# Performance work log

Measured on AMD Instinct MI355X. Metric: run time of the kernel, lower is better.

Reference implementation:

```python
import jax, jax.numpy as jnp
import numpy as np

N = 100000
F_IN = 128
HIDDEN = 64
HEADS = 4
EPS = 1e-16
SLOPE = 0.2  # PyG GATConv default negative_slope


def gat_conv(x, src, dst, W, a_src, a_dst, b, heads, out_ch, concat, n_nodes):
    # x: [N, F]; W: [F, heads*out_ch]; a_src/a_dst: [heads, out_ch]
    h = (x @ W).reshape(n_nodes, heads, out_ch)              # [N, H, C]
    alpha_s = jnp.einsum('nhc,hc->nh', h, a_src)             # [N, H]
    alpha_d = jnp.einsum('nhc,hc->nh', h, a_dst)             # [N, H]
    e = alpha_s[src] + alpha_d[dst]                          # [E, H]
    e = jnp.where(e > 0, e, SLOPE * e)                       # leaky_relu
    # segment softmax over destination node
    m = jax.ops.segment_max(e, dst, num_segments=n_nodes)    # [N, H]
    m = jnp.where(jnp.isfinite(m), m, 0.0)                   # empty segments
    ex = jnp.exp(e - m[dst])                                 # [E, H]
    denom = jax.ops.segment_sum(ex, dst, num_segments=n_nodes)  # [N, H]
    alpha = ex / (denom[dst] + EPS)                          # [E, H]
    # weighted scatter-aggregate of source features at destinations
    msg = h[src] * alpha[:, :, None]                         # [E, H, C]
    out = jax.ops.segment_sum(msg, dst, num_segments=n_nodes)  # [N, H, C]
    if concat:
        out = out.reshape(n_nodes, heads * out_ch)
    else:
        out = out.mean(axis=1)
    return out + b


def setup_inputs() -> dict:
    key = jax.random.key(0)
    ks = jax.random.split(key, 12)
    x = jax.random.normal(ks[0], (N, F_IN), dtype=jnp.float32)
    edge_index = jax.random.randint(ks[1], (2, 1600000), 0, N, dtype=jnp.int64)
    s1 = 1.0 / np.sqrt(F_IN)
    s2 = 1.0 / np.sqrt(HIDDEN)
    return {
        'x': x,
        'edge_index': edge_index,
        'W1': jax.random.normal(ks[2], (F_IN, HIDDEN), dtype=jnp.float32) * s1,
        'a_src1': jax.random.normal(ks[3], (HEADS, HIDDEN // HEADS), dtype=jnp.float32) * s2,
        'a_dst1': jax.random.normal(ks[4], (HEADS, HIDDEN // HEADS), dtype=jnp.float32) * s2,
        'b1': jnp.zeros((HIDDEN,), dtype=jnp.float32),
        'W2': jax.random.normal(ks[5], (HIDDEN, HIDDEN), dtype=jnp.float32) * s2,
        'a_src2': jax.random.normal(ks[6], (1, HIDDEN), dtype=jnp.float32) * s2,
        'a_dst2': jax.random.normal(ks[7], (1, HIDDEN), dtype=jnp.float32) * s2,
        'b2': jnp.zeros((HIDDEN,), dtype=jnp.float32),
        'Wc': jax.random.normal(ks[8], (HIDDEN, 1), dtype=jnp.float32) * s2,
        'bc': jnp.zeros((1,), dtype=jnp.float32),
    }


def reference(x, edge_index, W1, a_src1, a_dst1, b1, W2, a_src2, a_dst2, b2, Wc, bc):
    src, dst = edge_index[0], edge_index[1]
    # dropout layers are identity in eval mode
    h = gat_conv(x, src, dst, W1, a_src1, a_dst1, b1,
                 heads=HEADS, out_ch=HIDDEN // HEADS, concat=True, n_nodes=N)
    h = jax.nn.relu(h)
    h = gat_conv(h, src, dst, W2, a_src2, a_dst2, b2,
                 heads=1, out_ch=HIDDEN, concat=False, n_nodes=N)
    h = jax.nn.relu(h)
    return h @ Wc + bc  # [N, 1]
```

## Files before the change

kernel.cpp:

```cpp
#include <hip/hip_runtime.h>
#include <hip/hip_bf16.h>


typedef __hip_bfloat16 bf16;
typedef unsigned short ushort;
typedef unsigned char uchar;
typedef __attribute__((ext_vector_type(8))) short short8;
typedef __attribute__((ext_vector_type(4))) float f32x4;

#define NN 100000
#define EE 1600000
#define BKB 9
#define BKN (1 << BKB)
#define NBK ((NN + BKN - 1) >> BKB)
#define CAP 10240
#define TILE 4096
#define EPT 16
#define NT ((EE + TILE - 1) / TILE)
#define GH 391
#define GT 782
#define BN 16
#define CHE 512

__device__ __forceinline__ float relu_np(float v) { return (v < 0.f) ? 0.f : v; }
__device__ __forceinline__ float lrelu(float v) { return v > 0.f ? v : 0.2f * v; }
__device__ __forceinline__ ushort f2bf(float f) {
    __hip_bfloat16 h = __float2bfloat16(f);
    return *reinterpret_cast<ushort*>(&h);
}
__device__ __forceinline__ float bf2f(ushort u) {
    unsigned int x = ((unsigned int)u) << 16;
    return __uint_as_float(x);
}

__device__ __forceinline__ void gemm1_body(
    int gb, ushort* wB, ushort* wE,
    const float* __restrict__ x, const float* __restrict__ W1,
    const float* __restrict__ aS, const float* __restrict__ aD,
    ushort* __restrict__ h1, float* __restrict__ as1, float* __restrict__ ad1)
{
    const int tid = threadIdx.x;
    for (int i = tid; i < 128 * 64; i += 256) {
        int k = i >> 6, n = i & 63;
        wB[n * 128 + k] = f2bf(W1[i]);
    }
    for (int i = tid; i < 128 * 16; i += 256) {
        int k = i >> 4, j = i & 15;
        float v = 0.f;
        if (j < 8) {
            int h = j & 3;
            const float* av = (j < 4) ? aS : aD;
            for (int c = 0; c < 16; ++c)
                v = fmaf(W1[k * 64 + h * 16 + c], av[h * 16 + c], v);
        }
        wE[j * 128 + k] = f2bf(v);
    }
    __syncthreads();
    const int w = tid >> 6, lane = tid & 63;
    const int m = lane & 15, quad = lane >> 4;
    const int ntiles = NN >> 4;
    for (int tile = gb * 4 + w; tile < ntiles; tile += GT * 4) {
        const int row0 = tile << 4;
        f32x4 acc[4] = {f32x4{0,0,0,0}, f32x4{0,0,0,0},
                        f32x4{0,0,0,0}, f32x4{0,0,0,0}};
        f32x4 acc5 = {0, 0, 0, 0};
        const float* xp = x + (size_t)(row0 + m) * 128 + quad * 8;
        #pragma unroll
        for (int ks = 0; ks < 128; ks += 32) {
            f32x4 x0 = *(const f32x4*)(xp + ks);
            f32x4 x1 = *(const f32x4*)(xp + ks + 4);
            short8 a;
            #pragma unroll
            for (int j = 0; j < 4; ++j) a[j] = (short)f2bf(x0[j]);
            #pragma unroll
            for (int j = 0; j < 4; ++j) a[4 + j] = (short)f2bf(x1[j]);
            #pragma unroll
            for (int t = 0; t < 4; ++t) {
                short8 b = *(const short8*)&wB[(t * 16 + m) * 128 + ks + quad * 8];
                acc[t] = __builtin_amdgcn_mfma_f32_16x16x32_bf16(a, b, acc[t], 0, 0, 0);
            }
            short8 b5 = *(const short8*)&wE[m * 128 + ks + quad * 8];
            acc5 = __builtin_amdgcn_mfma_f32_16x16x32_bf16(a, b5, acc5, 0, 0, 0);
        }
        #pragma unroll
        for (int t = 0; t < 4; ++t)
            #pragma unroll
            for (int r = 0; r < 4; ++r)
                h1[(size_t)(row0 + quad * 4 + r) * 64 + t * 16 + m] = f2bf(acc[t][r]);
        #pragma unroll
        for (int r = 0; r < 4; ++r) {
            int row = row0 + quad * 4 + r;
            if (m < 4) as1[row * 4 + m] = acc5[r];
            else if (m < 8) ad1[row * 4 + (m - 4)] = acc5[r];
        }
    }
}

__global__ __launch_bounds__(256) void k_pg(
    const int* __restrict__ src, const int* __restrict__ dst,
    int* __restrict__ gcur, int* __restrict__ pairs,
    const float* __restrict__ x, const float* __restrict__ W1,
    const float* __restrict__ aS, const float* __restrict__ aD,
    ushort* __restrict__ h1, float* __restrict__ as1, float* __restrict__ ad1,
    const float* __restrict__ W2, const float* __restrict__ aS2,
    const float* __restrict__ aD2, ushort* __restrict__ wExt)
{
    __shared__ ushort wB[64 * 128];
    __shared__ ushort wE[16 * 128];
    __shared__ int lh[NBK];
    __shared__ int lbase[NBK];
    const int bid = blockIdx.x;
    const int tid = threadIdx.x;

    if (bid < NT) {
        for (int i = tid; i < NBK; i += 256) lh[i] = 0;
        __syncthreads();
        const int e0 = bid * TILE;
        int pk[EPT], bk[EPT], rv[EPT];
        #pragma unroll
        for (int j = 0; j < EPT; ++j) {
            int e = e0 + j * 256 + tid;
            if (e < EE) {
                int d = dst[e];
                bk[j] = d >> BKB;
                pk[j] = src[e] | ((d & (BKN - 1)) << 17);
                rv[j] = atomicAdd(&lh[bk[j]], 1);
            }
        }
        __syncthreads();
        for (int i = tid; i < NBK; i += 256)
            lbase[i] = lh[i] ? atomicAdd(&gcur[i], lh[i]) : 0;
        __syncthreads();
        #pragma unroll
        for (int j = 0; j < EPT; ++j) {
            int e = e0 + j * 256 + tid;
            if (e < EE)
                pairs[(size_t)bk[j] * CAP + lbase[bk[j]] + rv[j]] = pk[j];
        }
    } else if (bid < NT + GH) {
        gemm1_body(bid - NT, wB, wE, x, W1, aS, aD, h1, as1, ad1);
    } else {
        for (int i = tid; i < 80 * 64; i += 256) {
            int n = i >> 6, k = i & 63;
            float v = 0.f;
            if (n < 64) {
                v = W2[k * 64 + n];
            } else if (n == 64) {
                for (int c = 0; c < 64; ++c) v = fmaf(W2[k * 64 + c], aS2[c], v);
            } else if (n == 65) {
                for (int c = 0; c < 64; ++c) v = fmaf(W2[k * 64 + c], aD2[c], v);
            }
            wExt[i] = f2bf(v);
        }
    }
}

__global__ __launch_bounds__(256) void k_bg(
    const int* __restrict__ gcur, const int* __restrict__ pairs,
    int* __restrict__ row_ptr, uchar* __restrict__ rcnt,
    int* __restrict__ col,
    const float* __restrict__ x, const float* __restrict__ W1,
    const float* __restrict__ aS, const float* __restrict__ aD,
    ushort* __restrict__ h1, float* __restrict__ as1, float* __restrict__ ad1)
{
    __shared__ ushort wB[64 * 128];
    __shared__ ushort wE[16 * 128];
    __shared__ int hist[BKN];
    __shared__ int sP[256];
    const int bid = blockIdx.x;
    const int tid = threadIdx.x;

    if (bid >= NBK) {
        gemm1_body(bid - NBK + GH, wB, wE, x, W1, aS, aD, h1, as1, ad1);
        return;
    }

    const int b = bid;
    const int n0 = b << BKB;
    const int base = b * CAP, endE = base + gcur[b];
    for (int i = tid; i < BKN; i += 256) hist[i] = 0;
    __syncthreads();
    for (int i = base + tid; i < endE; i += 256)
        atomicAdd(&hist[pairs[i] >> 17], 1);
    __syncthreads();
    int a0 = hist[2 * tid], a1 = hist[2 * tid + 1];
    int tot = a0 + a1;
    sP[tid] = tot;
    __syncthreads();
    for (int off = 1; off < 256; off <<= 1) {
        int t = (tid >= off) ? sP[tid - off] : 0;
        __syncthreads();
        sP[tid] += t;
        __syncthreads();
    }
    const int excl = sP[tid] - tot;
    const int c0 = base + excl;
    hist[2 * tid] = c0;
    hist[2 * tid + 1] = c0 + a0;
    if (n0 + 2 * tid < NN) {
        row_ptr[n0 + 2 * tid] = c0;
        rcnt[n0 + 2 * tid] = (uchar)a0;
    }
    if (n0 + 2 * tid + 1 < NN) {
        row_ptr[n0 + 2 * tid + 1] = c0 + a0;
        rcnt[n0 + 2 * tid + 1] = (uchar)a1;
    }
    __syncthreads();
    for (int i = base + tid; i < endE; i += 256) {
        int pr = pairs[i];
        int p = atomicAdd(&hist[pr >> 17], 1);
        col[p] = pr & 0x1FFFF;
    }
}

__global__ __launch_bounds__(256, 8) void k_seg1f(
    const int* __restrict__ rp, const uchar* __restrict__ rcnt,
    const int* __restrict__ col,
    const float* __restrict__ as1, const float* __restrict__ ad1,
    const ushort* __restrict__ h1, const float* __restrict__ b1,
    const ushort* __restrict__ wExt,
    ushort* __restrict__ h2, float* __restrict__ as2, float* __restrict__ ad2,
    int N)
{
    __shared__ __align__(16) ushort zS[BN * 72];
    __shared__ float pS[CHE * 4];
    __shared__ int colS[CHE];
    __shared__ uchar ndS[CHE];
    __shared__ int sRp[BN + 1];
    __shared__ float bS[64];
    __shared__ float adS[BN * 4];

    const int tid = threadIdx.x;
    const int n0 = blockIdx.x * BN;

    if (tid < 64) bS[tid] = b1[tid];
    if (tid < BN * 4) adS[tid] = ad1[(size_t)n0 * 4 + tid];
    if (tid < BN) sRp[tid] = rp[n0 + tid];
    if (tid == BN) sRp[BN] = rp[n0 + BN - 1] + (int)rcnt[n0 + BN - 1];
    __syncthreads();

    const int eb0 = sRp[0];
    const int cnt = min(sRp[BN] - eb0, CHE);

    for (int t = tid; t < cnt; t += 256) {
        int ge = eb0 + t;
        colS[t] = col[ge];
        int nd = 0;
        #pragma unroll
        for (int k = 1; k < BN; ++k) nd += (ge >= sRp[k]);
        ndS[t] = (uchar)nd;
    }
    __syncthreads();
    for (int t = tid; t < cnt * 4; t += 256) {
        int e = t >> 2, hh = t & 3;
        float v = as1[(size_t)colS[e] * 4 + hh] + adS[ndS[e] * 4 + hh];
        pS[t] = __expf(lrelu(v));
    }
    __syncthreads();

    const int w = tid >> 6, lane = tid & 63;
    const int g = lane >> 4, c4 = lane & 15, head = c4 >> 2;
    const int nb = w * 4 + g;
    const int s_n = sRp[nb] - eb0, e_n = sRp[nb + 1] - eb0;

    f32x4 acc = {0, 0, 0, 0};
    float den = 0.f;
    int i = s_n;
    for (; i + 3 < e_n; i += 4) {
        int cA = colS[i], cB = colS[i + 1], cC = colS[i + 2], cD = colS[i + 3];
        ushort4 hA = *(const ushort4*)&h1[(size_t)cA * 64 + c4 * 4];
        ushort4 hB = *(const ushort4*)&h1[(size_t)cB * 64 + c4 * 4];
        ushort4 hC = *(const ushort4*)&h1[(size_t)cC * 64 + c4 * 4];
        ushort4 hD = *(const ushort4*)&h1[(size_t)cD * 64 + c4 * 4];
        float pA = pS[(i + 0) * 4 + head], pB = pS[(i + 1) * 4 + head];
        float pC = pS[(i + 2) * 4 + head], pD = pS[(i + 3) * 4 + head];
        den += (pA + pB) + (pC + pD);
        acc[0] = fmaf(pA, bf2f(hA.x), acc[0]);
        acc[1] = fmaf(pA, bf2f(hA.y), acc[1]);
        acc[2] = fmaf(pA, bf2f(hA.z), acc[2]);
        acc[3] = fmaf(pA, bf2f(hA.w), acc[3]);
        acc[0] = fmaf(pB, bf2f(hB.x), acc[0]);
        acc[1] = fmaf(pB, bf2f(hB.y), acc[1]);
        acc[2] = fmaf(pB, bf2f(hB.z), acc[2]);
        acc[3] = fmaf(pB, bf2f(hB.w), acc[3]);
        acc[0] = fmaf(pC, bf2f(hC.x), acc[0]);
        acc[1] = fmaf(pC, bf2f(hC.y), acc[1]);
        acc[2] = fmaf(pC, bf2f(hC.z), acc[2]);
        acc[3] = fmaf(pC, bf2f(hC.w), acc[3]);
        acc[0] = fmaf(pD, bf2f(hD.x), acc[0]);
        acc[1] = fmaf(pD, bf2f(hD.y), acc[1]);
        acc[2] = fmaf(pD, bf2f(hD.z), acc[2]);
        acc[3] = fmaf(pD, bf2f(hD.w), acc[3]);
    }
    for (; i < e_n; ++i) {
        int cA = colS[i];
        ushort4 hA = *(const ushort4*)&h1[(size_t)cA * 64 + c4 * 4];
        float pA = pS[i * 4 + head];
        den += pA;
        acc[0] = fmaf(pA, bf2f(hA.x), acc[0]);
        acc[1] = fmaf(pA, bf2f(hA.y), acc[1]);
        acc[2] = fmaf(pA, bf2f(hA.z), acc[2]);
        acc[3] = fmaf(pA, bf2f(hA.w), acc[3]);
    }
    {
        float inv = 1.f / (den + 1e-16f);
        ushort4 zv;
        zv.x = f2bf(relu_np(acc[0] * inv + bS[c4 * 4 + 0]));
        zv.y = f2bf(relu_np(acc[1] * inv + bS[c4 * 4 + 1]));
        zv.z = f2bf(relu_np(acc[2] * inv + bS[c4 * 4 + 2]));
        zv.w = f2bf(relu_np(acc[3] * inv + bS[c4 * 4 + 3]));
        *(ushort4*)&zS[nb * 72 + c4 * 4] = zv;
    }
    __syncthreads();

    const int m = c4, quad = g;
    for (int t = w; t < 5; t += 4) {
        f32x4 acct = {0, 0, 0, 0};
        #pragma unroll
        for (int ks = 0; ks < 64; ks += 32) {
            short8 a = *(const short8*)&zS[m * 72 + ks + quad * 8];
            short8 b = *(const short8*)&wExt[(t * 16 + m) * 64 + ks + quad * 8];
            acct = __builtin_amdgcn_mfma_f32_16x16x32_bf16(a, b, acct, 0, 0, 0);
        }
        if (t < 4) {
            #pragma unroll
            for (int r = 0; r < 4; ++r)
                h2[(size_t)(n0 + quad * 4 + r) * 64 + t * 16 + m] = f2bf(acct[r]);
        } else {
            #pragma unroll
            for (int r = 0; r < 4; ++r) {
                int row = n0 + quad * 4 + r;
                if (m == 0) as2[row] = acct[r];
                else if (m == 1) ad2[row] = acct[r];
            }
        }
    }
}

__global__ __launch_bounds__(256, 8) void k_seg2f(
    const int* __restrict__ rp, const uchar* __restrict__ rcnt,
    const int* __restrict__ col,
    const float* __restrict__ as2, const float* __restrict__ ad2,
    const ushort* __restrict__ h2, const float* __restrict__ b2,
    const float* __restrict__ Wc, const float* __restrict__ bc,
    float* __restrict__ out, int N)
{
    __shared__ float pS[CHE];
    __shared__ int colS[CHE];
    __shared__ uchar ndS[CHE];
    __shared__ int sRp[BN + 1];
    __shared__ float adS[BN];
    __shared__ float b2S[64];
    __shared__ float wcS[64];

    const int tid = threadIdx.x;
    const int n0 = blockIdx.x * BN;
    if (tid < 64) { b2S[tid] = b2[tid]; wcS[tid] = Wc[tid]; }
    if (tid < BN) { sRp[tid] = rp[n0 + tid]; adS[tid] = ad2[n0 + tid]; }
    if (tid == BN) sRp[BN] = rp[n0 + BN - 1] + (int)rcnt[n0 + BN - 1];
    __syncthreads();

    const int eb0 = sRp[0];
    const int cnt = min(sRp[BN] - eb0, CHE);
    for (int t = tid; t < cnt; t += 256) {
        int ge = eb0 + t;
        colS[t] = col[ge];
        int nd = 0;
        #pragma unroll
        for (int k = 1; k < BN; ++k) nd += (ge >= sRp[k]);
        ndS[t] = (uchar)nd;
    }
    __syncthreads();
    for (int t = tid; t < cnt; t += 256)
        pS[t] = __expf(lrelu(as2[colS[t]] + adS[ndS[t]]));
    __syncthreads();

    const int w = tid >> 6, lane = tid & 63;
    const int g = lane >> 4, c4 = lane & 15;
    const int nb = w * 4 + g;
    const int myn = n0 + nb;
    const int s_n = sRp[nb] - eb0, e_n = sRp[nb + 1] - eb0;

    f32x4 acc = {0, 0, 0, 0};
    float den = 0.f;
    int i = s_n;
    for (; i + 3 < e_n; i += 4) {
        int cA = colS[i], cB = colS[i + 1], cC = colS[i + 2], cD = colS[i + 3];
        ushort4 hA = *(const ushort4*)&h2[(size_t)cA * 64 + c4 * 4];
        ushort4 hB = *(const ushort4*)&h2[(size_t)cB * 64 + c4 * 4];
        ushort4 hC = *(const ushort4*)&h2[(size_t)cC * 64 + c4 * 4];
        ushort4 hD = *(const ushort4*)&h2[(size_t)cD * 64 + c4 * 4];
        float pA = pS[i + 0], pB = pS[i + 1], pC = pS[i + 2], pD = pS[i + 3];
        den += (pA + pB) + (pC + pD);
        acc[0] = fmaf(pA, bf2f(hA.x), acc[0]);
        acc[1] = fmaf(pA, bf2f(hA.y), acc[1]);
        acc[2] = fmaf(pA, bf2f(hA.z), acc[2]);
        acc[3] = fmaf(pA, bf2f(hA.w), acc[3]);
        acc[0] = fmaf(pB, bf2f(hB.x), acc[0]);
        acc[1] = fmaf(pB, bf2f(hB.y), acc[1]);
        acc[2] = fmaf(pB, bf2f(hB.z), acc[2]);
        acc[3] = fmaf(pB, bf2f(hB.w), acc[3]);
        acc[0] = fmaf(pC, bf2f(hC.x), acc[0]);
        acc[1] = fmaf(pC, bf2f(hC.y), acc[1]);
        acc[2] = fmaf(pC, bf2f(hC.z), acc[2]);
        acc[3] = fmaf(pC, bf2f(hC.w), acc[3]);
        acc[0] = fmaf(pD, bf2f(hD.x), acc[0]);
        acc[1] = fmaf(pD, bf2f(hD.y), acc[1]);
        acc[2] = fmaf(pD, bf2f(hD.z), acc[2]);
        acc[3] = fmaf(pD, bf2f(hD.w), acc[3]);
    }
    for (; i < e_n; ++i) {
        int cA = colS[i];
        ushort4 hA = *(const ushort4*)&h2[(size_t)cA * 64 + c4 * 4];
        float pA = pS[i];
        den += pA;
        acc[0] = fmaf(pA, bf2f(hA.x), acc[0]);
        acc[1] = fmaf(pA, bf2f(hA.y), acc[1]);
        acc[2] = fmaf(pA, bf2f(hA.z), acc[2]);
        acc[3] = fmaf(pA, bf2f(hA.w), acc[3]);
    }

    float inv = 1.f / (den + 1e-16f);
    float t2 = 0.f;
    #pragma unroll
    for (int j = 0; j < 4; ++j)
        t2 += relu_np(acc[j] * inv + b2S[c4 * 4 + j]) * wcS[c4 * 4 + j];
    t2 += __shfl_xor(t2, 1);
    t2 += __shfl_xor(t2, 2);
    t2 += __shfl_xor(t2, 4);
    t2 += __shfl_xor(t2, 8);
    if (c4 == 0) out[myn] = t2 + bc[0];
}

extern "C" void kernel_launch(void* const* d_in, const int* in_sizes, int n_in,
                              void* d_out, int out_size, void* d_ws, size_t ws_size,
                              hipStream_t stream)
{
    const float* x   = (const float*)d_in[0];
    const int*   ei  = (const int*)d_in[1];
    const float* W1  = (const float*)d_in[2];
    const float* aS1 = (const float*)d_in[3];
    const float* aD1 = (const float*)d_in[4];
    const float* b1  = (const float*)d_in[5];
    const float* W2  = (const float*)d_in[6];
    const float* aS2 = (const float*)d_in[7];
    const float* aD2 = (const float*)d_in[8];
    const float* b2  = (const float*)d_in[9];
    const float* Wc  = (const float*)d_in[10];
    const float* bc  = (const float*)d_in[11];
    float* out = (float*)d_out;

    const int N = NN;
    const int E = EE;
    const int* src = ei;
    const int* dst = ei + E;

    ushort* h1   = (ushort*)d_ws;
    ushort* h2   = h1 + (size_t)N * 64;
    float*  as1  = (float*)(h2 + (size_t)N * 64);
    float*  ad1  = as1 + (size_t)N * 4;
    float*  as2  = ad1 + (size_t)N * 4;
    float*  ad2  = as2 + (size_t)N;
    ushort* wExt = (ushort*)(ad2 + (size_t)N);
    int* row_ptr = (int*)(wExt + 80 * 64);
    uchar* rcnt  = (uchar*)(row_ptr + N);
    int* gcur    = (int*)(rcnt + ((N + 3) & ~3));
    int* col     = gcur + NBK;
    int* pairs   = (int*)h2;

    hipMemsetAsync(gcur, 0, NBK * sizeof(int), stream);

    k_pg<<<NT + GH + 1, 256, 0, stream>>>(src, dst, gcur, pairs,
                                          x, W1, aS1, aD1, h1, as1, ad1,
                                          W2, aS2, aD2, wExt);

    k_bg<<<NBK + GH, 256, 0, stream>>>(gcur, pairs, row_ptr, rcnt, col,
                                       x, W1, aS1, aD1, h1, as1, ad1);

    k_seg1f<<<N / BN, 256, 0, stream>>>(row_ptr, rcnt, col, as1, ad1, h1, b1,
                                        wExt, h2, as2, ad2, N);

    k_seg2f<<<N / BN, 256, 0, stream>>>(row_ptr, rcnt, col, as2, ad2, h2,
                                        b2, Wc, bc, out, N);
}
```

Measured before the change: 252.6 us.

## Precompute bf16 weights once, move whole GEMM1 into partition kernel, per-wave histograms

Adds a one-block prep kernel that zeroes the bucket counters and converts W1, the attention projections and W2 to bf16 in global memory once. This removes the memset and the per-block weight conversion into shared memory. All of GEMM1 now runs in the edge-partition kernel (391 GEMM blocks) instead of being split between the partition and bucket-sort kernels, so the bucket-sort kernel only sorts. The shared-memory atomic histograms in both the partition and bucket-sort stages become per-wave copies to cut atomic contention. In exchange, GEMM1 reads B fragments from global/L2 instead of LDS, and the new serial prep launch sits ahead of everything else.

New measurement: 255.4 us. About the same (+1.1%).

```diff
diff --git a/kernel.cpp b/kernel.cpp
--- a/kernel.cpp
+++ b/kernel.cpp
@@ -17,10 +17,10 @@
 #define TILE 4096
 #define EPT 16
 #define NT ((EE + TILE - 1) / TILE)
-#define GH 391
-#define GT 782
+#define GP 391
 #define BN 16
 #define CHE 512
+#define NGRP (NN / BN)
 
 __device__ __forceinline__ float relu_np(float v) { return (v < 0.f) ? 0.f : v; }
 __device__ __forceinline__ float lrelu(float v) { return v > 0.f ? v : 0.2f * v; }
@@ -33,88 +33,60 @@
     return __uint_as_float(x);
 }
 
-__device__ __forceinline__ void gemm1_body(
-    int gb, ushort* wB, ushort* wE,
-    const float* __restrict__ x, const float* __restrict__ W1,
-    const float* __restrict__ aS, const float* __restrict__ aD,
-    ushort* __restrict__ h1, float* __restrict__ as1, float* __restrict__ ad1)
+__global__ __launch_bounds__(256) void k_prep(
+    int* __restrict__ gcur, const float* __restrict__ W1,
+    const float* __restrict__ aS1, const float* __restrict__ aD1,
+    const float* __restrict__ W2, const float* __restrict__ aS2,
+    const float* __restrict__ aD2,
+    ushort* __restrict__ wB16, ushort* __restrict__ wE16,
+    ushort* __restrict__ wExt)
 {
     const int tid = threadIdx.x;
+    if (tid < NBK) gcur[tid] = 0;
     for (int i = tid; i < 128 * 64; i += 256) {
         int k = i >> 6, n = i & 63;
-        wB[n * 128 + k] = f2bf(W1[i]);
+        wB16[n * 128 + k] = f2bf(W1[i]);
     }
     for (int i = tid; i < 128 * 16; i += 256) {
         int k = i >> 4, j = i & 15;
         float v = 0.f;
         if (j < 8) {
             int h = j & 3;
-            const float* av = (j < 4) ? aS : aD;
+            const float* av = (j < 4) ? aS1 : aD1;
             for (int c = 0; c < 16; ++c)
                 v = fmaf(W1[k * 64 + h * 16 + c], av[h * 16 + c], v);
         }
-        wE[j * 128 + k] = f2bf(v);
-    }
-    __syncthreads();
-    const int w = tid >> 6, lane = tid & 63;
-    const int m = lane & 15, quad = lane >> 4;
-    const int ntiles = NN >> 4;
-    for (int tile = gb * 4 + w; tile < ntiles; tile += GT * 4) {
-        const int row0 = tile << 4;
-        f32x4 acc[4] = {f32x4{0,0,0,0}, f32x4{0,0,0,0},
-                        f32x4{0,0,0,0}, f32x4{0,0,0,0}};
-        f32x4 acc5 = {0, 0, 0, 0};
-        const float* xp = x + (size_t)(row0 + m) * 128 + quad * 8;
-        #pragma unroll
-        for (int ks = 0; ks < 128; ks += 32) {
-            f32x4 x0 = *(const f32x4*)(xp + ks);
-            f32x4 x1 = *(const f32x4*)(xp + ks + 4);
-            short8 a;
-            #pragma unroll
-            for (int j = 0; j < 4; ++j) a[j] = (short)f2bf(x0[j]);
-            #pragma unroll
-            for (int j = 0; j < 4; ++j) a[4 + j] = (short)f2bf(x1[j]);
-            #pragma unroll
-            for (int t = 0; t < 4; ++t) {
-                short8 b = *(const short8*)&wB[(t * 16 + m) * 128 + ks + quad * 8];
-                acc[t] = __builtin_amdgcn_mfma_f32_16x16x32_bf16(a, b, acc[t], 0, 0, 0);
-            }
-            short8 b5 = *(const short8*)&wE[m * 128 + ks + quad * 8];
-            acc5 = __builtin_amdgcn_mfma_f32_16x16x32_bf16(a, b5, acc5, 0, 0, 0);
-        }
-        #pragma unroll
-        for (int t = 0; t < 4; ++t)
-            #pragma unroll
-            for (int r = 0; r < 4; ++r)
-                h1[(size_t)(row0 + quad * 4 + r) * 64 + t * 16 + m] = f2bf(acc[t][r]);
-        #pragma unroll
-        for (int r = 0; r < 4; ++r) {
-            int row = row0 + quad * 4 + r;
-            if (m < 4) as1[row * 4 + m] = acc5[r];
-            else if (m < 8) ad1[row * 4 + (m - 4)] = acc5[r];
-        }
+        wE16[j * 128 + k] = f2bf(v);
+    }
+    for (int i = tid; i < 80 * 64; i += 256) {
+        int n = i >> 6, k = i & 63;
+        float v = 0.f;
+        if (n < 64) {
+            v = W2[k * 64 + n];
+        } else if (n == 64) {
+            for (int c = 0; c < 64; ++c) v = fmaf(W2[k * 64 + c], aS2[c], v);
+        } else if (n == 65) {
+            for (int c = 0; c < 64; ++c) v = fmaf(W2[k * 64 + c], aD2[c], v);
+        }
+        wExt[i] = f2bf(v);
     }
 }
 
 __global__ __launch_bounds__(256) void k_pg(
     const int* __restrict__ src, const int* __restrict__ dst,
     int* __restrict__ gcur, int* __restrict__ pairs,
-    const float* __restrict__ x, const float* __restrict__ W1,
-    const float* __restrict__ aS, const float* __restrict__ aD,
-    ushort* __restrict__ h1, float* __restrict__ as1, float* __restrict__ ad1,
-    const float* __restrict__ W2, const float* __restrict__ aS2,
-    const float* __restrict__ aD2, ushort* __restrict__ wExt)
-{
-    __shared__ ushort wB[64 * 128];
-    __shared__ ushort wE[16 * 128];
-    __shared__ int lh[NBK];
-    __shared__ int lbase[NBK];
+    const float* __restrict__ x,
+    const ushort* __restrict__ wB16, const ushort* __restrict__ wE16,
+    ushort* __restrict__ h1, float* __restrict__ as1, float* __restrict__ ad1)
+{
+    __shared__ int lh[4][NBK];
     const int bid = blockIdx.x;
     const int tid = threadIdx.x;
 
     if (bid < NT) {
-        for (int i = tid; i < NBK; i += 256) lh[i] = 0;
+        for (int i = tid; i < 4 * NBK; i += 256) ((int*)lh)[i] = 0;
         __syncthreads();
+        const int wv = tid >> 6;
         const int e0 = bid * TILE;
         int pk[EPT], bk[EPT], rv[EPT];
         #pragma unroll
@@ -124,33 +96,65 @@
                 int d = dst[e];
                 bk[j] = d >> BKB;
                 pk[j] = src[e] | ((d & (BKN - 1)) << 17);
-                rv[j] = atomicAdd(&lh[bk[j]], 1);
+                rv[j] = atomicAdd(&lh[wv][bk[j]], 1);
             }
         }
         __syncthreads();
-        for (int i = tid; i < NBK; i += 256)
-            lbase[i] = lh[i] ? atomicAdd(&gcur[i], lh[i]) : 0;
+        for (int i = tid; i < NBK; i += 256) {
+            int c0 = lh[0][i], c1 = lh[1][i], c2 = lh[2][i], c3 = lh[3][i];
+            int tot = c0 + c1 + c2 + c3;
+            int b = tot ? atomicAdd(&gcur[i], tot) : 0;
+            lh[0][i] = b;
+            lh[1][i] = b + c0;
+            lh[2][i] = b + c0 + c1;
+            lh[3][i] = b + c0 + c1 + c2;
+        }
         __syncthreads();
         #pragma unroll
         for (int j = 0; j < EPT; ++j) {
             int e = e0 + j * 256 + tid;
             if (e < EE)
-                pairs[(size_t)bk[j] * CAP + lbase[bk[j]] + rv[j]] = pk[j];
-        }
-    } else if (bid < NT + GH) {
-        gemm1_body(bid - NT, wB, wE, x, W1, aS, aD, h1, as1, ad1);
+                pairs[(size_t)bk[j] * CAP + lh[wv][bk[j]] + rv[j]] = pk[j];
+        }
     } else {
-        for (int i = tid; i < 80 * 64; i += 256) {
-            int n = i >> 6, k = i & 63;
-            float v = 0.f;
-            if (n < 64) {
-                v = W2[k * 64 + n];
-            } else if (n == 64) {
-                for (int c = 0; c < 64; ++c) v = fmaf(W2[k * 64 + c], aS2[c], v);
-            } else if (n == 65) {
-                for (int c = 0; c < 64; ++c) v = fmaf(W2[k * 64 + c], aD2[c], v);
+        const int gb = bid - NT;
+        const int w = tid >> 6, lane = tid & 63;
+        const int m = lane & 15, quad = lane >> 4;
+        const int ntiles = NN >> 4;
+        for (int tile = gb * 4 + w; tile < ntiles; tile += GP * 4) {
+            const int row0 = tile << 4;
+            f32x4 acc[4] = {f32x4{0,0,0,0}, f32x4{0,0,0,0},
+                            f32x4{0,0,0,0}, f32x4{0,0,0,0}};
+            f32x4 acc5 = {0, 0, 0, 0};
+            const float* xp = x + (size_t)(row0 + m) * 128 + quad * 8;
+            #pragma unroll
+            for (int ks = 0; ks < 128; ks += 32) {
+                f32x4 x0 = *(const f32x4*)(xp + ks);
+                f32x4 x1 = *(const f32x4*)(xp + ks + 4);
+                short8 a;
+                #pragma unroll
+                for (int j = 0; j < 4; ++j) a[j] = (short)f2bf(x0[j]);
+                #pragma unroll
+                for (int j = 0; j < 4; ++j) a[4 + j] = (short)f2bf(x1[j]);
+                #pragma unroll
+                for (int t = 0; t < 4; ++t) {
+                    short8 b = *(const short8*)&wB16[(t * 16 + m) * 128 + ks + quad * 8];
+                    acc[t] = __builtin_amdgcn_mfma_f32_16x16x32_bf16(a, b, acc[t], 0, 0, 0);
+                }
+                short8 b5 = *(const short8*)&wE16[m * 128 + ks + quad * 8];
+                acc5 = __builtin_amdgcn_mfma_f32_16x16x32_bf16(a, b5, acc5, 0, 0, 0);
             }
-            wExt[i] = f2bf(v);
+            #pragma unroll
+            for (int t = 0; t < 4; ++t)
+                #pragma unroll
+                for (int r = 0; r < 4; ++r)
+                    h1[(size_t)(row0 + quad * 4 + r) * 64 + t * 16 + m] = f2bf(acc[t][r]);
+            #pragma unroll
+            for (int r = 0; r < 4; ++r) {
+                int row = row0 + quad * 4 + r;
+                if (m < 4) as1[row * 4 + m] = acc5[r];
+                else if (m < 8) ad1[row * 4 + (m - 4)] = acc5[r];
+            }
         }
     }
 }
@@ -158,32 +162,27 @@
 __global__ __launch_bounds__(256) void k_bg(
     const int* __restrict__ gcur, const int* __restrict__ pairs,
     int* __restrict__ row_ptr, uchar* __restrict__ rcnt,
-    int* __restrict__ col,
-    const float* __restrict__ x, const float* __restrict__ W1,
-    const float* __restrict__ aS, const float* __restrict__ aD,
-    ushort* __restrict__ h1, float* __restrict__ as1, float* __restrict__ ad1)
-{
-    __shared__ ushort wB[64 * 128];
-    __shared__ ushort wE[16 * 128];
-    __shared__ int hist[BKN];
+    int* __restrict__ col)
+{
+    __shared__ int h4[4][BKN];
     __shared__ int sP[256];
-    const int bid = blockIdx.x;
+    const int b = blockIdx.x;
+    const int n0 = b << BKB;
     const int tid = threadIdx.x;
-
-    if (bid >= NBK) {
-        gemm1_body(bid - NBK + GH, wB, wE, x, W1, aS, aD, h1, as1, ad1);
-        return;
-    }
-
-    const int b = bid;
-    const int n0 = b << BKB;
+    const int wv = tid >> 6;
     const int base = b * CAP, endE = base + gcur[b];
-    for (int i = tid; i < BKN; i += 256) hist[i] = 0;
+
+    for (int i = tid; i < 4 * BKN; i += 256) ((int*)h4)[i] = 0;
     __syncthreads();
     for (int i = base + tid; i < endE; i += 256)
-        atomicAdd(&hist[pairs[i] >> 17], 1);
-    __syncthreads();
-    int a0 = hist[2 * tid], a1 = hist[2 * tid + 1];
+        atomicAdd(&h4[wv][pairs[i] >> 17], 1);
+    __syncthreads();
+
+    const int na = 2 * tid, nb2 = 2 * tid + 1;
+    int c00 = h4[0][na], c01 = h4[1][na], c02 = h4[2][na], c03 = h4[3][na];
+    int c10 = h4[0][nb2], c11 = h4[1][nb2], c12 = h4[2][nb2], c13 = h4[3][nb2];
+    int a0 = c00 + c01 + c02 + c03;
+    int a1 = c10 + c11 + c12 + c13;
     int tot = a0 + a1;
     sP[tid] = tot;
     __syncthreads();
@@ -195,20 +194,27 @@
     }
     const int excl = sP[tid] - tot;
     const int c0 = base + excl;
-    hist[2 * tid] = c0;
-    hist[2 * tid + 1] = c0 + a0;
-    if (n0 + 2 * tid < NN) {
-        row_ptr[n0 + 2 * tid] = c0;
-        rcnt[n0 + 2 * tid] = (uchar)a0;
-    }
-    if (n0 + 2 * tid + 1 < NN) {
-        row_ptr[n0 + 2 * tid + 1] = c0 + a0;
-        rcnt[n0 + 2 * tid + 1] = (uchar)a1;
-    }
+    const int c1 = c0 + a0;
+    if (n0 + na < NN) {
+        row_ptr[n0 + na] = c0;
+        rcnt[n0 + na] = (uchar)a0;
+    }
+    if (n0 + nb2 < NN) {
+        row_ptr[n0 + nb2] = c1;
+        rcnt[n0 + nb2] = (uchar)a1;
+    }
+    h4[0][na] = c0;
+    h4[1][na] = c0 + c00;
+    h4[2][na] = c0 + c00 + c01;
+    h4[3][na] = c0 + c00 + c01 + c02;
+    h4[0][nb2] = c1;
+    h4[1][nb2] = c1 + c10;
+    h4[2][nb2] = c1 + c10 + c11;
+    h4[3][nb2] = c1 + c10 + c11 + c12;
     __syncthreads();
     for (int i = base + tid; i < endE; i += 256) {
         int pr = pairs[i];
-        int p = atomicAdd(&hist[pr >> 17], 1);
+        int p = atomicAdd(&h4[wv][pr >> 17], 1);
         col[p] = pr & 0x1FFFF;
     }
 }
@@ -219,8 +225,7 @@
     const float* __restrict__ as1, const float* __restrict__ ad1,
     const ushort* __restrict__ h1, const float* __restrict__ b1,
     const ushort* __restrict__ wExt,
-    ushort* __restrict__ h2, float* __restrict__ as2, float* __restrict__ ad2,
-    int N)
+    ushort* __restrict__ h2, float* __restrict__ as2, float* __restrict__ ad2)
 {
     __shared__ __align__(16) ushort zS[BN * 72];
     __shared__ float pS[CHE * 4];
@@ -343,7 +348,7 @@
     const float* __restrict__ as2, const float* __restrict__ ad2,
     const ushort* __restrict__ h2, const float* __restrict__ b2,
     const float* __restrict__ Wc, const float* __restrict__ bc,
-    float* __restrict__ out, int N)
+    float* __restrict__ out)
 {
     __shared__ float pS[CHE];
     __shared__ int colS[CHE];
@@ -450,36 +455,35 @@
     const float* bc  = (const float*)d_in[11];
     float* out = (float*)d_out;
 
-    const int N = NN;
-    const int E = EE;
     const int* src = ei;
-    const int* dst = ei + E;
+    const int* dst = ei + EE;
 
     ushort* h1   = (ushort*)d_ws;
-    ushort* h2   = h1 + (size_t)N * 64;
-    float*  as1  = (float*)(h2 + (size_t)N * 64);
-    float*  ad1  = as1 + (size_t)N * 4;
-    float*  as2  = ad1 + (size_t)N * 4;
-    float*  ad2  = as2 + (size_t)N;
-    ushort* wExt = (ushort*)(ad2 + (size_t)N);
-    int* row_ptr = (int*)(wExt + 80 * 64);
-    uchar* rcnt  = (uchar*)(row_ptr + N);
-    int* gcur    = (int*)(rcnt + ((N + 3) & ~3));
+    ushort* h2   = h1 + (size_t)NN * 64;
+    float*  as1  = (float*)(h2 + (size_t)NN * 64);
+    float*  ad1  = as1 + (size_t)NN * 4;
+    float*  as2  = ad1 + (size_t)NN * 4;
+    float*  ad2  = as2 + (size_t)NN;
+    ushort* wExt = (ushort*)(ad2 + (size_t)NN);
+    ushort* wB16 = wExt + 80 * 64;
+    ushort* wE16 = wB16 + 64 * 128;
+    int* row_ptr = (int*)(wE16 + 16 * 128);
+    uchar* rcnt  = (uchar*)(row_ptr + NN);
+    int* gcur    = (int*)(rcnt + ((NN + 3) & ~3));
     int* col     = gcur + NBK;
     int* pairs   = (int*)h2;
 
-    hipMemsetAsync(gcur, 0, NBK * sizeof(int), stream);
-
-    k_pg<<<NT + GH + 1, 256, 0, stream>>>(src, dst, gcur, pairs,
-                                          x, W1, aS1, aD1, h1, as1, ad1,
-                                          W2, aS2, aD2, wExt);
-
-    k_bg<<<NBK + GH, 256, 0, stream>>>(gcur, pairs, row_ptr, rcnt, col,
-                                       x, W1, aS1, aD1, h1, as1, ad1);
-
-    k_seg1f<<<N / BN, 256, 0, stream>>>(row_ptr, rcnt, col, as1, ad1, h1, b1,
-                                        wExt, h2, as2, ad2, N);
-
-    k_seg2f<<<N / BN, 256, 0, stream>>>(row_ptr, rcnt, col, as2, ad2, h2,
-                                        b2, Wc, bc, out, N);
-}
+    k_prep<<<1, 256, 0, stream>>>(gcur, W1, aS1, aD1, W2, aS2, aD2,
+                                  wB16, wE16, wExt);
+
+    k_pg<<<NT + GP, 256, 0, stream>>>(src, dst, gcur, pairs, x,
+                                      wB16, wE16, h1, as1, ad1);
+
+    k_bg<<<NBK, 256, 0, stream>>>(gcur, pairs, row_ptr, rcnt, col);
+
+    k_seg1f<<<NGRP, 256, 0, stream>>>(row_ptr, rcnt, col, as1, ad1, h1, b1,
+                                      wExt, h2, as2, ad2);
+
+    k_seg2f<<<NGRP, 256, 0, stream>>>(row_ptr, rcnt, col, as2, ad2, h2,
+                                      b2, Wc, bc, out);
+}
```
